# Optimization experiments

Measured on AMD Instinct MI355X. Metric: run time of the kernel, lower is better.

The kernel has to match this reference:

```python
import jax, jax.numpy as jnp
import numpy as np

N_NODES = 50000
N_EDGES = 1_600_000
NUM_GRAPHS = 64
F_NODE = 32
F_EDGE = 16
H = 64
L = 3
BN_EPS = 1e-5


def setup_inputs() -> dict:
    key = jax.random.key(0)
    ks = jax.random.split(key, 20)
    x = jax.random.normal(ks[0], (N_NODES, F_NODE), jnp.float32)
    edge_attr = jax.random.normal(ks[1], (N_EDGES, F_EDGE), jnp.float32)
    edge_index = jax.random.randint(ks[2], (2, N_EDGES), 0, N_NODES, dtype=jnp.int64)
    batch = jnp.sort(jax.random.randint(ks[3], (N_NODES,), 0, NUM_GRAPHS, dtype=jnp.int64))

    def lin(k, fan_in, shape):
        return jax.random.normal(k, shape, jnp.float32) * (1.0 / np.sqrt(fan_in))

    node_W = lin(ks[4], F_NODE, (F_NODE, H));  node_b = jnp.zeros((H,), jnp.float32)
    edge_W = lin(ks[5], F_EDGE, (F_EDGE, H));  edge_b = jnp.zeros((H,), jnp.float32)
    # GINE per-layer MLP: Linear(H, 2H) -> ReLU -> Linear(2H, H)
    W1s = lin(ks[6], H, (L, H, 2 * H));   b1s = jnp.zeros((L, 2 * H), jnp.float32)
    W2s = lin(ks[7], 2 * H, (L, 2 * H, H)); b2s = jnp.zeros((L, H), jnp.float32)
    gammas = jnp.ones((L, H), jnp.float32)
    betas = jnp.zeros((L, H), jnp.float32)
    lin_W = lin(ks[8], H, (H, 1));  lin_b = jnp.zeros((1,), jnp.float32)
    return {
        "x": x, "edge_attr": edge_attr, "edge_index": edge_index, "batch": batch,
        "node_W": node_W, "node_b": node_b, "edge_W": edge_W, "edge_b": edge_b,
        "W1s": W1s, "b1s": b1s, "W2s": W2s, "b2s": b2s,
        "gammas": gammas, "betas": betas, "lin_W": lin_W, "lin_b": lin_b,
    }


def reference(x, edge_attr, edge_index, batch, node_W, node_b, edge_W, edge_b,
              W1s, b1s, W2s, b2s, gammas, betas, lin_W, lin_b):
    # node / edge embeddings
    h = x @ node_W + node_b                  # [N, H]
    e = edge_attr @ edge_W + edge_b          # [E, H]
    src, dst = edge_index[0], edge_index[1]
    for l in range(L):
        # GINEConv (eps=0): m_ij = relu(x_j + e_ij), aggregate sum at target
        m = jax.nn.relu(h[src] + e)                                  # [E, H]
        agg = jax.ops.segment_sum(m, dst, num_segments=N_NODES)     # [N, H]
        z = h + agg
        z = jax.nn.relu(z @ W1s[l] + b1s[l]) @ W2s[l] + b2s[l]       # GINE MLP
        # BatchNorm (training-mode batch stats, biased variance) + ReLU
        mu = jnp.mean(z, axis=0)
        var = jnp.var(z, axis=0)
        h = jax.nn.relu(gammas[l] * (z - mu) * jax.lax.rsqrt(var + BN_EPS) + betas[l])
    # global mean pool per graph
    counts = jax.ops.segment_sum(jnp.ones((N_NODES,), h.dtype), batch, num_segments=NUM_GRAPHS)
    gsum = jax.ops.segment_sum(h, batch, num_segments=NUM_GRAPHS)   # [G, H]
    graph_x = gsum / jnp.maximum(counts, 1.0)[:, None]
    return graph_x @ lin_W + lin_b                                   # [G, 1]
```

## Files before the change

kernel.cpp:

```cpp
#include <hip/hip_runtime.h>

#define NN 50000
#define NE 1600000
#define NG 64
#define HD 64
#define BN_EPS 1e-5f
#define NTILES ((NN + 31) / 32)

typedef unsigned short ushort_t;
typedef unsigned int uint_t;
typedef __attribute__((ext_vector_type(8))) short bf16x8;
typedef __attribute__((ext_vector_type(4))) float f32x4;

__device__ __forceinline__ float b2f(ushort_t u) {
  union { uint_t i; float f; } v; v.i = ((uint_t)u) << 16; return v.f;
}
__device__ __forceinline__ ushort_t f2b(float f) {
  union { float f; uint_t i; } v; v.f = f;
  uint_t x = v.i;
  return (ushort_t)((x + 0x7fffu + ((x >> 16) & 1u)) >> 16);
}
__device__ __forceinline__ uint_t packsplit(float f) {
  ushort_t hi = f2b(f);
  float r = f - b2f(hi);
  ushort_t lo = f2b(r);
  return (uint_t)hi | ((uint_t)lo << 16);
}
__device__ __forceinline__ float LDF(const void* p, int i, int isb) {
  return isb ? b2f(((const ushort_t*)p)[i]) : ((const float*)p)[i];
}
__device__ __forceinline__ int LDI(const void* p, int i, int is64) {
  return is64 ? ((const int*)p)[2 * i] : ((const int*)p)[i];
}
__device__ __forceinline__ int clampi(int v, int hi) {
  return (v < 0) ? 0 : (v >= hi ? hi - 1 : v);
}

__global__ void detect_k(const uint_t* __restrict__ xw, const uint_t* __restrict__ ew,
                         int* __restrict__ flags) {
  int t = threadIdx.x;
  uint_t w = xw[t];
  uint_t b = (w >> 8) & 0x7fu;
  unsigned long long m1 = __ballot(b >= 0x3au && b <= 0x42u);
  unsigned long long m2 = __ballot(ew[2 * t + 1] == 0u);
  if (t == 0) {
    flags[0] = (__popcll(m1) >= 32) ? 1 : 0;
    flags[1] = (__popcll(m2) >= 56) ? 1 : 0;
  }
}

__global__ void __launch_bounds__(256) node_embed(
    const void* __restrict__ x, const void* __restrict__ W,
    const void* __restrict__ b, float* __restrict__ h, const int* __restrict__ flags) {
  __shared__ float xs[64 * 32];
  int isb = flags[0];
  int t = threadIdx.x;
  int base = blockIdx.x * 64;
  int nodes = NN - base; if (nodes > 64) nodes = 64;
  int idx = t * 8;
  if (idx < nodes * 32) {
    if (isb) {
      const uint4* p = (const uint4*)((const ushort_t*)x + base * 32);
      uint4 u = p[t];
      ushort_t* pu = (ushort_t*)&u;
      #pragma unroll
      for (int q = 0; q < 8; q++) xs[idx + q] = b2f(pu[q]);
    } else {
      const float4* p = (const float4*)((const float*)x + base * 32);
      float4 a = p[2 * t], d = p[2 * t + 1];
      xs[idx + 0] = a.x; xs[idx + 1] = a.y; xs[idx + 2] = a.z; xs[idx + 3] = a.w;
      xs[idx + 4] = d.x; xs[idx + 5] = d.y; xs[idx + 6] = d.z; xs[idx + 7] = d.w;
    }
  }
  int c = t & 63, s0 = t >> 6;
  float w[32];
  #pragma unroll
  for (int k = 0; k < 32; k++) w[k] = LDF(W, k * 64 + c, isb);
  float bc = LDF(b, c, isb);
  __syncthreads();
  #pragma unroll 4
  for (int i = 0; i < 16; i++) {
    int slot = s0 * 16 + i;
    int node = base + slot;
    if (node < NN) {
      float acc = bc;
      #pragma unroll
      for (int k = 0; k < 32; k++) acc += xs[slot * 32 + k] * w[k];
      h[node * 64 + c] = acc;
    }
  }
}

__global__ void __launch_bounds__(256) hist_k(
    const void* __restrict__ eidx, int* __restrict__ hist, const int* __restrict__ flags) {
  int is64 = flags[1];
  int e = blockIdx.x * 256 + threadIdx.x;
  if (e >= NE) return;
  int d = clampi(LDI(eidx, NE + e, is64), NN);
  atomicAdd(&hist[d], 1);
}

__global__ void __launch_bounds__(1024) scan_k(
    const int* __restrict__ hist, int* __restrict__ offs) {
  __shared__ int buf[1024];
  int t = threadIdx.x;
  int beg = t * 49, end = beg + 49; if (end > NN) end = NN; if (beg > NN) beg = NN;
  int s = 0;
  for (int i = beg; i < end; i++) s += hist[i];
  buf[t] = s;
  __syncthreads();
  for (int d = 1; d < 1024; d <<= 1) {
    int x = (t >= d) ? buf[t - d] : 0;
    __syncthreads();
    buf[t] += x;
    __syncthreads();
  }
  int run = buf[t] - s;
  for (int i = beg; i < end; i++) { int hv = hist[i]; offs[i] = run; run += hv; }
  if (t == 1023) offs[NN] = run;
}

__global__ void __launch_bounds__(256) scatter_k(
    const void* __restrict__ eidx, int* __restrict__ cursor,
    int* __restrict__ perm, int* __restrict__ psrc, int* __restrict__ pdst,
    const int* __restrict__ flags) {
  int is64 = flags[1];
  int e = blockIdx.x * 256 + threadIdx.x;
  if (e >= NE) return;
  int d = clampi(LDI(eidx, NE + e, is64), NN);
  int s = clampi(LDI(eidx, e, is64), NN);
  int pos = atomicAdd(&cursor[d], 1);
  perm[pos] = e;
  psrc[pos] = s;
  pdst[pos] = d;
}

__global__ void __launch_bounds__(256) pack_eattr(
    const void* __restrict__ eattr, const int* __restrict__ perm,
    ushort_t* __restrict__ phi, ushort_t* __restrict__ plo,
    const int* __restrict__ flags) {
  int isb = flags[0];
  int pos = blockIdx.x * 256 + threadIdx.x;
  if (pos >= NE) return;
  int e = perm[pos];
  int tile = pos >> 4, r = pos & 15;
  union U8 { ushort_t s[8]; uint4 u; };
  if (isb) {
    const uint4* p = (const uint4*)((const ushort_t*)eattr + (size_t)e * 16);
    uint4 h0 = p[0], h1 = p[1];
    ((uint4*)phi)[tile * 32 + r] = h0;
    ((uint4*)phi)[tile * 32 + 16 + r] = h1;
  } else {
    const float4* p = (const float4*)((const float*)eattr + (size_t)e * 16);
    U8 hi[2], lo[2];
    #pragma unroll
    for (int q = 0; q < 4; q++) {
      float4 v = p[q];
      float vv[4] = {v.x, v.y, v.z, v.w};
      #pragma unroll
      for (int j = 0; j < 4; j++) {
        int idx = q * 4 + j;
        ushort_t hb = f2b(vv[j]);
        hi[idx >> 3].s[idx & 7] = hb;
        lo[idx >> 3].s[idx & 7] = f2b(vv[j] - b2f(hb));
      }
    }
    ((uint4*)phi)[tile * 32 + r] = hi[0].u;
    ((uint4*)phi)[tile * 32 + 16 + r] = hi[1].u;
    ((uint4*)plo)[tile * 32 + r] = lo[0].u;
    ((uint4*)plo)[tile * 32 + 16 + r] = lo[1].u;
  }
}

__global__ void __launch_bounds__(256) edge_mfma(
    const ushort_t* __restrict__ phi, const ushort_t* __restrict__ plo,
    const int* __restrict__ psrc, const int* __restrict__ pdst,
    const uint4* __restrict__ wfrag, const float* __restrict__ h,
    float* __restrict__ agg, const int* __restrict__ flags) {
  __shared__ float es[64 * 65];
  __shared__ int ss[64], sd[64];
  int isb = flags[0];
  int t = threadIdx.x;
  int base = blockIdx.x * 64;
  if (t < 64) ss[t] = psrc[base + t];
  else if (t < 128) sd[t - 64] = pdst[base + t - 64];
  int w = t >> 6, lane = t & 63, kg = lane >> 4, cr = lane & 15;
  int tile = blockIdx.x * 4 + w;
  union FR { uint4 u; bf16x8 v; };
  FR ahi, alo;
  ahi.u = make_uint4(0u, 0u, 0u, 0u);
  alo.u = ahi.u;
  if (kg < 2) {
    ahi.u = ((const uint4*)phi)[tile * 32 + kg * 16 + cr];
    if (!isb) alo.u = ((const uint4*)plo)[tile * 32 + kg * 16 + cr];
  }
  f32x4 acc[4];
  #pragma unroll
  for (int nt = 0; nt < 4; nt++) acc[nt] = (f32x4){0.f, 0.f, 0.f, 0.f};
  #pragma unroll
  for (int nt = 0; nt < 4; nt++) {
    FR bh; bh.u = wfrag[nt * 64 + lane];
    acc[nt] = __builtin_amdgcn_mfma_f32_16x16x32_bf16(ahi.v, bh.v, acc[nt], 0, 0, 0);
    if (!isb) {
      FR bl; bl.u = wfrag[256 + nt * 64 + lane];
      acc[nt] = __builtin_amdgcn_mfma_f32_16x16x32_bf16(ahi.v, bl.v, acc[nt], 0, 0, 0);
      acc[nt] = __builtin_amdgcn_mfma_f32_16x16x32_bf16(alo.v, bh.v, acc[nt], 0, 0, 0);
    }
  }
  const float* ebias = (const float*)(wfrag + 512);
  #pragma unroll
  for (int nt = 0; nt < 4; nt++) {
    float bv = ebias[nt * 16 + cr];
    #pragma unroll
    for (int r = 0; r < 4; r++)
      es[(w * 16 + kg * 4 + r) * 65 + nt * 16 + cr] = acc[nt][r] + bv;
  }
  __syncthreads();
  int c = lane, s0 = w;
  float accr = 0.f;
  int cur = -1;
  for (int i = 0; i < 16; i++) {
    int slot = s0 * 16 + i;
    int sn = ss[slot], dn = sd[slot];
    float m = h[(size_t)sn * 64 + c] + es[slot * 65 + c];
    m = m > 0.f ? m : 0.f;
    if (dn != cur) {
      if (cur >= 0) atomicAdd(&agg[cur * 64 + c], accr);
      cur = dn; accr = 0.f;
    }
    accr += m;
  }
  if (cur >= 0) atomicAdd(&agg[cur * 64 + c], accr);
}

__global__ void __launch_bounds__(256) edge_sorted(
    const void* __restrict__ eattr, const int* __restrict__ perm,
    const int* __restrict__ psrc, const int* __restrict__ pdst,
    const void* __restrict__ eW, const void* __restrict__ eb,
    const float* __restrict__ h, float* __restrict__ agg, const int* __restrict__ flags) {
  __shared__ float ea[64 * 16];
  __shared__ int ss[64], sd[64];
  int isb = flags[0];
  int t = threadIdx.x;
  int base = blockIdx.x * 64;
  if (t < 64) ss[t] = psrc[base + t];
  else if (t < 128) sd[t - 64] = pdst[base + t - 64];
  {
    int slot = t >> 2, q = t & 3;
    int pe = perm[base + slot];
    if (isb) {
      const uint2* p = (const uint2*)((const ushort_t*)eattr + (size_t)pe * 16 + q * 4);
      uint2 u = *p;
      ea[slot * 16 + q * 4 + 0] = b2f((ushort_t)(u.x & 0xffffu));
      ea[slot * 16 + q * 4 + 1] = b2f((ushort_t)(u.x >> 16));
      ea[slot * 16 + q * 4 + 2] = b2f((ushort_t)(u.y & 0xffffu));
      ea[slot * 16 + q * 4 + 3] = b2f((ushort_t)(u.y >> 16));
    } else {
      const float4* p = (const float4*)((const float*)eattr + (size_t)pe * 16 + q * 4);
      float4 v = *p;
      ea[slot * 16 + q * 4 + 0] = v.x;
      ea[slot * 16 + q * 4 + 1] = v.y;
      ea[slot * 16 + q * 4 + 2] = v.z;
      ea[slot * 16 + q * 4 + 3] = v.w;
    }
  }
  int c = t & 63, s0 = t >> 6;
  float w[16];
  #pragma unroll
  for (int k = 0; k < 16; k++) w[k] = LDF(eW, k * 64 + c, isb);
  float bc = LDF(eb, c, isb);
  __syncthreads();
  float acc = 0.f;
  int cur = -1;
  for (int i = 0; i < 16; i++) {
    int slot = s0 * 16 + i;
    int sn = ss[slot], dn = sd[slot];
    float e = bc;
    #pragma unroll
    for (int k = 0; k < 16; k++) e += ea[slot * 16 + k] * w[k];
    float m = h[sn * 64 + c] + e;
    m = m > 0.f ? m : 0.f;
    if (dn != cur) {
      if (cur >= 0) atomicAdd(&agg[cur * 64 + c], acc);
      cur = dn; acc = 0.f;
    }
    acc += m;
  }
  if (cur >= 0) atomicAdd(&agg[cur * 64 + c], acc);
}

__global__ void __launch_bounds__(256) prep_w(
    const void* __restrict__ W1s, const void* __restrict__ W2s,
    const void* __restrict__ eW, const void* __restrict__ eB,
    uint4* __restrict__ wpk, const int* __restrict__ flags) {
  int l = blockIdx.x, t = threadIdx.x, isb = flags[0];
  union U8 { ushort_t s[8]; uint4 u; };
  if (l == 3) {
    uint4* wfrag = wpk + 3 * 4096;
    int nt = t >> 6, lane = t & 63;
    int col = nt * 16 + (lane & 15);
    U8 hi, lo;
    #pragma unroll
    for (int j = 0; j < 8; j++) {
      int k = (lane >> 4) * 8 + j;
      float wf = (k < 16) ? LDF(eW, k * 64 + col, isb) : 0.f;
      ushort_t hb = f2b(wf);
      hi.s[j] = hb;
      lo.s[j] = f2b(wf - b2f(hb));
    }
    wfrag[nt * 64 + lane] = hi.u;
    wfrag[256 + nt * 64 + lane] = lo.u;
    if (t < 64) ((float*)(wfrag + 512))[t] = LDF(eB, t, isb);
    return;
  }
  uint4* w1hi = wpk + (size_t)l * 4096;
  uint4* w1lo = w1hi + 1024;
  uint4* w2hi = w1hi + 2048;
  uint4* w2lo = w1hi + 3072;
  for (int o = t; o < 1024; o += 256) {
    int lane = o & 63, f = (o >> 6) & 7, hh = o >> 9;
    int q = lane >> 4, m = lane & 15;
    {
      int kc = f >> 2, i = f & 3;
      U8 hi, lo;
      #pragma unroll
      for (int j = 0; j < 8; j++) {
        int idx = l * 8192 + (kc * 32 + q * 8 + j) * 128 + (hh * 4 + i) * 16 + m;
        float wf = LDF(W1s, idx, isb);
        ushort_t hb = f2b(wf);
        hi.s[j] = hb;
        lo.s[j] = f2b(wf - b2f(hb));
      }
      w1hi[o] = hi.u;
      w1lo[o] = lo.u;
    }
    {
      int kc = f >> 1, i = f & 1;
      U8 hi, lo;
      #pragma unroll
      for (int j = 0; j < 8; j++) {
        int idx = l * 8192 + (kc * 32 + q * 8 + j) * 64 + (hh * 2 + i) * 16 + m;
        float wf = LDF(W2s, idx, isb);
        ushort_t hb = f2b(wf);
        hi.s[j] = hb;
        lo.s[j] = f2b(wf - b2f(hb));
      }
      w2hi[o] = hi.u;
      w2lo[o] = lo.u;
    }
  }
}

__global__ void __launch_bounds__(256) mlp_mfma(
    const float* __restrict__ h, const float* agg,
    const uint4* __restrict__ wpk, const void* __restrict__ b1s,
    const void* __restrict__ b2s,
    float* z2out, float* __restrict__ bnsum, const int* __restrict__ flags, int layer) {
  __shared__ uint_t zs[32 * 65];
  __shared__ uint_t a1s[32 * 129];
  int isb = flags[0];
  int t = threadIdx.x;
  int w = t >> 6, lane = t & 63, q = lane >> 4, m = lane & 15;
  int mt = w & 1;
  int hh = w >> 1;
  int ng1 = hh * 4;
  int ng2 = hh * 2;
  int b1off = layer * 128, b2off = layer * 64;
  const uint4* w1hi = wpk + (size_t)layer * 4096;
  const uint4* w1lo = w1hi + 1024;
  const uint4* w2hi = w1hi + 2048;
  const uint4* w2lo = w1hi + 3072;

  union FR { uint4 u; bf16x8 v; };
  FR w1f[4][2], w2f[2][4];
  #pragma unroll
  for (int kc = 0; kc < 2; kc++)
    #pragma unroll
    for (int i = 0; i < 4; i++)
      w1f[i][kc].u = w1hi[(hh * 8 + kc * 4 + i) * 64 + lane];
  #pragma unroll
  for (int kc = 0; kc < 4; kc++)
    #pragma unroll
    for (int i = 0; i < 2; i++)
      w2f[i][kc].u = w2hi[(hh * 8 + kc * 2 + i) * 64 + lane];

  float b1v[4], b2v[2];
  #pragma unroll
  for (int i = 0; i < 4; i++) b1v[i] = LDF(b1s, b1off + (ng1 + i) * 16 + m, isb);
  #pragma unroll
  for (int i = 0; i < 2; i++) b2v[i] = LDF(b2s, b2off + (ng2 + i) * 16 + m, isb);

  int srow = t >> 3, scol = (t & 7) * 8;
  float ps[2] = {0.f, 0.f}, pq[2] = {0.f, 0.f};

  for (int tile = blockIdx.x; tile < NTILES; tile += gridDim.x) {
    int base = tile * 32;
    __syncthreads();
    {
      int gr = base + srow;
      if (gr < NN) {
        const float4* hp = (const float4*)(h + (size_t)gr * 64 + scol);
        const float4* ap = (const float4*)(agg + (size_t)gr * 64 + scol);
        float4 h0 = hp[0], h1 = hp[1], a0 = ap[0], a1 = ap[1];
        zs[srow * 65 + scol + 0] = packsplit(h0.x + a0.x);
        zs[srow * 65 + scol + 1] = packsplit(h0.y + a0.y);
        zs[srow * 65 + scol + 2] = packsplit(h0.z + a0.z);
        zs[srow * 65 + scol + 3] = packsplit(h0.w + a0.w);
        zs[srow * 65 + scol + 4] = packsplit(h1.x + a1.x);
        zs[srow * 65 + scol + 5] = packsplit(h1.y + a1.y);
        zs[srow * 65 + scol + 6] = packsplit(h1.z + a1.z);
        zs[srow * 65 + scol + 7] = packsplit(h1.w + a1.w);
      } else {
        #pragma unroll
        for (int jj = 0; jj < 8; jj++) zs[srow * 65 + scol + jj] = 0;
      }
    }
    __syncthreads();
    f32x4 acc1[4];
    #pragma unroll
    for (int i = 0; i < 4; i++) acc1[i] = (f32x4){0.f, 0.f, 0.f, 0.f};
    #pragma unroll
    for (int kc = 0; kc < 2; kc++) {
      int ab = (mt * 16 + m) * 65 + kc * 32 + q * 8;
      bf16x8 ahi, alo;
      #pragma unroll
      for (int j = 0; j < 8; j++) {
        uint_t u = zs[ab + j];
        ahi[j] = (short)(u & 0xffffu);
        alo[j] = (short)(u >> 16);
      }
      #pragma unroll
      for (int i = 0; i < 4; i++) {
        acc1[i] = __builtin_amdgcn_mfma_f32_16x16x32_bf16(ahi, w1f[i][kc].v, acc1[i], 0, 0, 0);
        acc1[i] = __builtin_amdgcn_mfma_f32_16x16x32_bf16(alo, w1f[i][kc].v, acc1[i], 0, 0, 0);
        if (!isb) {
          FR bl;
          bl.u = w1lo[(hh * 8 + kc * 4 + i) * 64 + lane];
          acc1[i] = __builtin_amdgcn_mfma_f32_16x16x32_bf16(ahi, bl.v, acc1[i], 0, 0, 0);
        }
      }
    }
    #pragma unroll
    for (int i = 0; i < 4; i++) {
      #pragma unroll
      for (int r = 0; r < 4; r++) {
        float v = acc1[i][r] + b1v[i];
        v = v > 0.f ? v : 0.f;
        a1s[(mt * 16 + q * 4 + r) * 129 + (ng1 + i) * 16 + m] = packsplit(v);
      }
    }
    __syncthreads();
    f32x4 acc2[2];
    #pragma unroll
    for (int i = 0; i < 2; i++) acc2[i] = (f32x4){0.f, 0.f, 0.f, 0.f};
    #pragma unroll
    for (int kc = 0; kc < 4; kc++) {
      int ab = (mt * 16 + m) * 129 + kc * 32 + q * 8;
      bf16x8 ahi, alo;
      #pragma unroll
      for (int j = 0; j < 8; j++) {
        uint_t u = a1s[ab + j];
        ahi[j] = (short)(u & 0xffffu);
        alo[j] = (short)(u >> 16);
      }
      #pragma unroll
      for (int i = 0; i < 2; i++) {
        acc2[i] = __builtin_amdgcn_mfma_f32_16x16x32_bf16(ahi, w2f[i][kc].v, acc2[i], 0, 0, 0);
        acc2[i] = __builtin_amdgcn_mfma_f32_16x16x32_bf16(alo, w2f[i][kc].v, acc2[i], 0, 0, 0);
        if (!isb) {
          FR bl;
          bl.u = w2lo[(hh * 8 + kc * 2 + i) * 64 + lane];
          acc2[i] = __builtin_amdgcn_mfma_f32_16x16x32_bf16(ahi, bl.v, acc2[i], 0, 0, 0);
        }
      }
    }
    #pragma unroll
    for (int i = 0; i < 2; i++) {
      int col = (ng2 + i) * 16 + m;
      #pragma unroll
      for (int r = 0; r < 4; r++) {
        int gr = base + mt * 16 + q * 4 + r;
        if (gr < NN) {
          float v = acc2[i][r] + b2v[i];
          z2out[(size_t)gr * 64 + col] = v;
          ps[i] += v; pq[i] += v * v;
        }
      }
    }
  }
  __syncthreads();
  float* red = (float*)zs;
  if (t < 128) red[t] = 0.f;
  __syncthreads();
  #pragma unroll
  for (int i = 0; i < 2; i++) {
    int col = (ng2 + i) * 16 + m;
    atomicAdd(&red[col], ps[i]);
    atomicAdd(&red[64 + col], pq[i]);
  }
  __syncthreads();
  if (t < 128) atomicAdd(&bnsum[t], red[t]);
}

__global__ void bn_fin(const float* __restrict__ bnsum, const void* __restrict__ gammas,
                       const void* __restrict__ betas, float* __restrict__ scsh,
                       const int* __restrict__ flags, int layer) {
  int c = threadIdx.x;
  int isb = flags[0];
  float inv_n = 1.0f / (float)NN;
  float mu = bnsum[c] * inv_n;
  float var = bnsum[64 + c] * inv_n - mu * mu;
  var = var > 0.f ? var : 0.f;
  float sc = LDF(gammas, layer * 64 + c, isb) * rsqrtf(var + BN_EPS);
  scsh[c] = sc;
  scsh[64 + c] = LDF(betas, layer * 64 + c, isb) - mu * sc;
}

__global__ void __launch_bounds__(256) bn_apply(
    const float* __restrict__ z2, const float* __restrict__ scsh, float* __restrict__ h) {
  int t = blockIdx.x * 256 + threadIdx.x;
  if (t < NN * 16) {
    float4 z = ((const float4*)z2)[t];
    int c4 = t & 15;
    float4 sc = ((const float4*)scsh)[c4];
    float4 sh = ((const float4*)(scsh + 64))[c4];
    float4 r;
    r.x = fmaxf(z.x * sc.x + sh.x, 0.f);
    r.y = fmaxf(z.y * sc.y + sh.y, 0.f);
    r.z = fmaxf(z.z * sc.z + sh.z, 0.f);
    r.w = fmaxf(z.w * sc.w + sh.w, 0.f);
    ((float4*)h)[t] = r;
  }
}

__global__ void __launch_bounds__(256) find_bounds(
    const void* __restrict__ batch, int* __restrict__ bounds, const int* __restrict__ flags) {
  int is64 = flags[1];
  int i = blockIdx.x * 256 + threadIdx.x;
  if (i >= NN) return;
  int cur = clampi(LDI(batch, i, is64), NG);
  if (i == 0) {
    for (int g = 0; g <= cur; g++) bounds[g] = 0;
  } else {
    int prev = clampi(LDI(batch, i - 1, is64), NG);
    for (int g = prev + 1; g <= cur; g++) bounds[g] = i;
  }
  if (i == NN - 1) {
    for (int g = cur + 1; g <= NG; g++) bounds[g] = NN;
  }
}

__global__ void __launch_bounds__(256) pool_final(
    const float* __restrict__ h, const int* __restrict__ bounds,
    const void* __restrict__ linW, const void* __restrict__ linB,
    float* __restrict__ out, const int* __restrict__ flags) {
  __shared__ float red[4][64];
  int isb = flags[0];
  int g = blockIdx.x;
  int t = threadIdx.x, c = t & 63, w = t >> 6;
  int s = bounds[g], e = bounds[g + 1];
  float acc = 0.f;
  for (int i = s + w; i < e; i += 4) acc += h[i * 64 + c];
  red[w][c] = acc;
  __syncthreads();
  if (t < 64) {
    float v = red[0][c] + red[1][c] + red[2][c] + red[3][c];
    float cnt = (float)(e - s); if (cnt < 1.f) cnt = 1.f;
    v = (v / cnt) * LDF(linW, c, isb);
    #pragma unroll
    for (int m = 32; m >= 1; m >>= 1) v += __shfl_xor(v, m, 64);
    if (c == 0) out[g] = v + LDF(linB, 0, isb);
  }
}

extern "C" void kernel_launch(void* const* d_in, const int* in_sizes, int n_in,
                              void* d_out, int out_size, void* d_ws, size_t ws_size,
                              hipStream_t stream) {
  const void* x     = d_in[0];
  const void* eattr = d_in[1];
  const void* eidx  = d_in[2];
  const void* batch = d_in[3];
  const void* nodeW = d_in[4];
  const void* nodeB = d_in[5];
  const void* edgeW = d_in[6];
  const void* edgeB = d_in[7];
  const void* W1s   = d_in[8];
  const void* b1s   = d_in[9];
  const void* W2s   = d_in[10];
  const void* b2s   = d_in[11];
  const void* gam   = d_in[12];
  const void* bet   = d_in[13];
  const void* linW  = d_in[14];
  const void* linB  = d_in[15];
  float* out = (float*)d_out;

  int*   flags  = (int*)d_ws;
  float* h      = (float*)d_ws + 16;
  float* agg    = h + (size_t)NN * HD;
  float* bnsum  = agg + (size_t)NN * HD;
  float* scsh   = bnsum + 128;
  int*   bounds = (int*)(scsh + 128);
  int*   offs   = bounds + 80;
  int*   cursor = offs + (NN + 1);
  int*   perm   = cursor + (NN + 1);
  int*   psrc   = perm + NE;
  int*   pdst   = psrc + NE;

  size_t base_words = 16ull + 2ull * NN * HD + 128 + 128 + 80;
  size_t sort_words = base_words + 2ull * (NN + 1) + 3ull * NE;
  size_t wpk_words_start = (sort_words + 3ull) & ~3ull;
  size_t wpk_words = (3ull * 4096 + 528) * 4;
  size_t needed = (wpk_words_start + wpk_words) * 4ull;
  if (ws_size < needed) return;
  uint4* wpk = (uint4*)((float*)d_ws + wpk_words_start);
  uint4* wfrag = wpk + 3ull * 4096;
  size_t z2_start = wpk_words_start + wpk_words;
  float* z2sep = (float*)d_ws + z2_start;
  int have_z2 = ws_size >= (z2_start + (size_t)NN * HD) * 4ull;
  float* z2 = have_z2 ? z2sep : agg;
  size_t pat_start = z2_start + (size_t)NN * HD;
  size_t pat_words = (size_t)NE * 8;
  int have_pat = have_z2 && (ws_size >= (pat_start + 2ull * pat_words) * 4ull);
  ushort_t* phi = (ushort_t*)((float*)d_ws + pat_start);
  ushort_t* plo = (ushort_t*)((float*)d_ws + pat_start + pat_words);

  detect_k<<<1, 64, 0, stream>>>((const uint_t*)x, (const uint_t*)eidx, flags);
  prep_w<<<4, 256, 0, stream>>>(W1s, W2s, edgeW, edgeB, wpk, flags);
  node_embed<<<(NN + 63) / 64, 256, 0, stream>>>(x, nodeW, nodeB, h, flags);

  hipMemsetAsync(offs, 0, (NN + 1) * sizeof(int), stream);
  hist_k<<<NE / 256, 256, 0, stream>>>(eidx, offs, flags);
  scan_k<<<1, 1024, 0, stream>>>(offs, cursor);
  scatter_k<<<NE / 256, 256, 0, stream>>>(eidx, cursor, perm, psrc, pdst, flags);
  if (have_pat)
    pack_eattr<<<NE / 256, 256, 0, stream>>>(eattr, perm, phi, plo, flags);

  for (int l = 0; l < 3; l++) {
    hipMemsetAsync(agg, 0, (size_t)NN * HD * sizeof(float), stream);
    if (have_pat)
      edge_mfma<<<NE / 64, 256, 0, stream>>>(phi, plo, psrc, pdst, wfrag, h, agg, flags);
    else
      edge_sorted<<<NE / 64, 256, 0, stream>>>(eattr, perm, psrc, pdst, edgeW, edgeB, h, agg, flags);
    hipMemsetAsync(bnsum, 0, 128 * sizeof(float), stream);
    mlp_mfma<<<784, 256, 0, stream>>>(h, agg, wpk, b1s, b2s, z2, bnsum, flags, l);
    bn_fin<<<1, 64, 0, stream>>>(bnsum, gam, bet, scsh, flags, l);
    bn_apply<<<3125, 256, 0, stream>>>(z2, scsh, h);
  }
  find_bounds<<<(NN + 255) / 256, 256, 0, stream>>>(batch, bounds, flags);
  pool_final<<<NG, 256, 0, stream>>>(h, bounds, linW, linB, out, flags);
}
```

Measured before the change: 1.081 ms.

## Bucket edges by source range and pin buckets to XCDs for L2 locality

Edges are now sorted by a composite key of source-node bucket (8 buckets of 6250 nodes) and destination, and each bucket is padded to 64-edge chunks. The edge kernel maps blockIdx&7 to a bucket so each XCD gathers h rows from one source range, meant to keep those gathers resident in that XCD's L2. The per-thread h gathers are also hoisted into a register array so the loads can be issued together. In exchange, the histogram and scan work over 8x more bins, padding edges need masking, and destinations repeat across buckets, so segmented runs are shorter and more atomics are issued.

```diff
diff --git a/kernel.cpp b/kernel.cpp
--- a/kernel.cpp
+++ b/kernel.cpp
@@ -6,6 +6,11 @@
 #define HD 64
 #define BN_EPS 1e-5f
 #define NTILES ((NN + 31) / 32)
+#define NBUCK 8
+#define NPB 6250
+#define NBINS (NBUCK * NN)
+#define NEP (NE + 512)
+#define SLOTS 3584
 
 typedef unsigned short ushort_t;
 typedef unsigned int uint_t;
@@ -97,17 +102,48 @@
   int e = blockIdx.x * 256 + threadIdx.x;
   if (e >= NE) return;
   int d = clampi(LDI(eidx, NE + e, is64), NN);
-  atomicAdd(&hist[d], 1);
+  int s = clampi(LDI(eidx, e, is64), NN);
+  int bin = (s / NPB) * NN + d;
+  atomicAdd(&hist[bin], 1);
 }
 
 __global__ void __launch_bounds__(1024) scan_k(
-    const int* __restrict__ hist, int* __restrict__ offs) {
+    const int* __restrict__ hist, int* __restrict__ starts, int* __restrict__ meta) {
   __shared__ int buf[1024];
+  __shared__ int sA[NBUCK + 1];
+  __shared__ int sT[NBUCK];
+  __shared__ int sPT[NBUCK];
   int t = threadIdx.x;
-  int beg = t * 49, end = beg + 49; if (end > NN) end = NN; if (beg > NN) beg = NN;
-  int s = 0;
-  for (int i = beg; i < end; i++) s += hist[i];
-  buf[t] = s;
+  int active = t < 1000;
+  const int4* h4 = (const int4*)hist;
+  int4* s4 = (int4*)starts;
+  int ssum = 0;
+  if (active) {
+    for (int i = t * 100; i < t * 100 + 100; i++) {
+      int4 v = h4[i];
+      ssum += v.x + v.y + v.z + v.w;
+    }
+  }
+  buf[t] = ssum;
+  __syncthreads();
+  if (t < NBUCK) {
+    int T = 0;
+    for (int i = t * 125; i < t * 125 + 125; i++) T += buf[i];
+    sT[t] = T;
+  }
+  __syncthreads();
+  if (t == 0) {
+    int a = 0, pt = 0;
+    for (int b = 0; b < NBUCK; b++) {
+      sA[b] = a; sPT[b] = pt;
+      meta[b] = a;
+      meta[16 + b] = a + sT[b];
+      pt += sT[b];
+      a = (a + sT[b] + 63) & ~63;
+    }
+    sA[NBUCK] = a;
+    meta[NBUCK] = a;
+  }
   __syncthreads();
   for (int d = 1; d < 1024; d <<= 1) {
     int x = (t >= d) ? buf[t - d] : 0;
@@ -115,9 +151,30 @@
     buf[t] += x;
     __syncthreads();
   }
-  int run = buf[t] - s;
-  for (int i = beg; i < end; i++) { int hv = hist[i]; offs[i] = run; run += hv; }
-  if (t == 1023) offs[NN] = run;
+  if (active) {
+    int b = t / 125;
+    int run = sA[b] + (buf[t] - ssum - sPT[b]);
+    for (int i = t * 100; i < t * 100 + 100; i++) {
+      int4 v = h4[i];
+      int4 o;
+      o.x = run; run += v.x;
+      o.y = run; run += v.y;
+      o.z = run; run += v.z;
+      o.w = run; run += v.w;
+      s4[i] = o;
+    }
+  }
+}
+
+__global__ void pad_fill(const int* __restrict__ meta, int* __restrict__ perm,
+                         int* __restrict__ psrc, int* __restrict__ pdst) {
+  int t = threadIdx.x;
+  for (int b = 0; b < NBUCK; b++) {
+    int re = meta[16 + b], ae = meta[b + 1];
+    for (int p = re + t; p < ae; p += 64) {
+      perm[p] = 0; psrc[p] = 0; pdst[p] = NN;
+    }
+  }
 }
 
 __global__ void __launch_bounds__(256) scatter_k(
@@ -129,7 +186,8 @@
   if (e >= NE) return;
   int d = clampi(LDI(eidx, NE + e, is64), NN);
   int s = clampi(LDI(eidx, e, is64), NN);
-  int pos = atomicAdd(&cursor[d], 1);
+  int bin = (s / NPB) * NN + d;
+  int pos = atomicAdd(&cursor[bin], 1);
   perm[pos] = e;
   psrc[pos] = s;
   pdst[pos] = d;
@@ -138,10 +196,10 @@
 __global__ void __launch_bounds__(256) pack_eattr(
     const void* __restrict__ eattr, const int* __restrict__ perm,
     ushort_t* __restrict__ phi, ushort_t* __restrict__ plo,
-    const int* __restrict__ flags) {
+    const int* __restrict__ flags, const int* __restrict__ meta) {
   int isb = flags[0];
   int pos = blockIdx.x * 256 + threadIdx.x;
-  if (pos >= NE) return;
+  if (pos >= meta[8]) return;
   int e = perm[pos];
   int tile = pos >> 4, r = pos & 15;
   union U8 { ushort_t s[8]; uint4 u; };
@@ -176,16 +234,35 @@
     const ushort_t* __restrict__ phi, const ushort_t* __restrict__ plo,
     const int* __restrict__ psrc, const int* __restrict__ pdst,
     const uint4* __restrict__ wfrag, const float* __restrict__ h,
-    float* __restrict__ agg, const int* __restrict__ flags) {
-  __shared__ float es[64 * 65];
+    float* __restrict__ agg, const int* __restrict__ flags,
+    const int* __restrict__ meta) {
+  __shared__ float es[64 * 68];
   __shared__ int ss[64], sd[64];
+  int A[9];
+  #pragma unroll
+  for (int b = 0; b < 9; b++) A[b] = meta[b];
+  int maxcb = 0;
+  #pragma unroll
+  for (int b = 0; b < NBUCK; b++) {
+    int cb = (A[b + 1] - A[b]) >> 6;
+    maxcb = cb > maxcb ? cb : maxcb;
+  }
+  int chunk;
+  if (maxcb <= SLOTS) {
+    int xcd = blockIdx.x & 7, s = blockIdx.x >> 3;
+    if (s >= ((A[xcd + 1] - A[xcd]) >> 6)) return;
+    chunk = (A[xcd] >> 6) + s;
+  } else {
+    chunk = blockIdx.x;
+    if (chunk * 64 >= A[8]) return;
+  }
+  int base = chunk * 64;
   int isb = flags[0];
   int t = threadIdx.x;
-  int base = blockIdx.x * 64;
   if (t < 64) ss[t] = psrc[base + t];
   else if (t < 128) sd[t - 64] = pdst[base + t - 64];
   int w = t >> 6, lane = t & 63, kg = lane >> 4, cr = lane & 15;
-  int tile = blockIdx.x * 4 + w;
+  int tile = chunk * 4 + w;
   union FR { uint4 u; bf16x8 v; };
   FR ahi, alo;
   ahi.u = make_uint4(0u, 0u, 0u, 0u);
@@ -213,36 +290,43 @@
     float bv = ebias[nt * 16 + cr];
     #pragma unroll
     for (int r = 0; r < 4; r++)
-      es[(w * 16 + kg * 4 + r) * 65 + nt * 16 + cr] = acc[nt][r] + bv;
+      es[(w * 16 + kg * 4 + r) * 68 + nt * 16 + cr] = acc[nt][r] + bv;
   }
   __syncthreads();
   int c = lane, s0 = w;
+  float hv[16];
+  #pragma unroll
+  for (int i = 0; i < 16; i++)
+    hv[i] = h[(size_t)ss[s0 * 16 + i] * 64 + c];
   float accr = 0.f;
   int cur = -1;
+  #pragma unroll
   for (int i = 0; i < 16; i++) {
     int slot = s0 * 16 + i;
-    int sn = ss[slot], dn = sd[slot];
-    float m = h[(size_t)sn * 64 + c] + es[slot * 65 + c];
+    int dn = sd[slot];
+    float m = hv[i] + es[slot * 68 + c];
     m = m > 0.f ? m : 0.f;
     if (dn != cur) {
-      if (cur >= 0) atomicAdd(&agg[cur * 64 + c], accr);
+      if (cur >= 0 && cur < NN) atomicAdd(&agg[cur * 64 + c], accr);
       cur = dn; accr = 0.f;
     }
     accr += m;
   }
-  if (cur >= 0) atomicAdd(&agg[cur * 64 + c], accr);
+  if (cur >= 0 && cur < NN) atomicAdd(&agg[cur * 64 + c], accr);
 }
 
 __global__ void __launch_bounds__(256) edge_sorted(
     const void* __restrict__ eattr, const int* __restrict__ perm,
     const int* __restrict__ psrc, const int* __restrict__ pdst,
     const void* __restrict__ eW, const void* __restrict__ eb,
-    const float* __restrict__ h, float* __restrict__ agg, const int* __restrict__ flags) {
+    const float* __restrict__ h, float* __restrict__ agg,
+    const int* __restrict__ flags, const int* __restrict__ meta) {
   __shared__ float ea[64 * 16];
   __shared__ int ss[64], sd[64];
   int isb = flags[0];
   int t = threadIdx.x;
   int base = blockIdx.x * 64;
+  if (base >= meta[8]) return;
   if (t < 64) ss[t] = psrc[base + t];
   else if (t < 128) sd[t - 64] = pdst[base + t - 64];
   {
@@ -281,12 +365,12 @@
     float m = h[sn * 64 + c] + e;
     m = m > 0.f ? m : 0.f;
     if (dn != cur) {
-      if (cur >= 0) atomicAdd(&agg[cur * 64 + c], acc);
+      if (cur >= 0 && cur < NN) atomicAdd(&agg[cur * 64 + c], acc);
       cur = dn; acc = 0.f;
     }
     acc += m;
   }
-  if (cur >= 0) atomicAdd(&agg[cur * 64 + c], acc);
+  if (cur >= 0 && cur < NN) atomicAdd(&agg[cur * 64 + c], acc);
 }
 
 __global__ void __launch_bounds__(256) prep_w(
@@ -595,20 +679,21 @@
   float* out = (float*)d_out;
 
   int*   flags  = (int*)d_ws;
-  float* h      = (float*)d_ws + 16;
+  int*   meta   = flags + 16;
+  float* h      = (float*)(meta + 48);
   float* agg    = h + (size_t)NN * HD;
   float* bnsum  = agg + (size_t)NN * HD;
   float* scsh   = bnsum + 128;
   int*   bounds = (int*)(scsh + 128);
   int*   offs   = bounds + 80;
-  int*   cursor = offs + (NN + 1);
-  int*   perm   = cursor + (NN + 1);
-  int*   psrc   = perm + NE;
-  int*   pdst   = psrc + NE;
-
-  size_t base_words = 16ull + 2ull * NN * HD + 128 + 128 + 80;
-  size_t sort_words = base_words + 2ull * (NN + 1) + 3ull * NE;
-  size_t wpk_words_start = (sort_words + 3ull) & ~3ull;
+  int*   cursor = offs + NBINS;
+  int*   perm   = cursor + NBINS;
+  int*   psrc   = perm + NEP;
+  int*   pdst   = psrc + NEP;
+
+  size_t base_words = 64ull + 2ull * NN * HD + 128 + 128 + 80
+                    + 2ull * NBINS + 3ull * NEP;
+  size_t wpk_words_start = (base_words + 3ull) & ~3ull;
   size_t wpk_words = (3ull * 4096 + 528) * 4;
   size_t needed = (wpk_words_start + wpk_words) * 4ull;
   if (ws_size < needed) return;
@@ -619,7 +704,7 @@
   int have_z2 = ws_size >= (z2_start + (size_t)NN * HD) * 4ull;
   float* z2 = have_z2 ? z2sep : agg;
   size_t pat_start = z2_start + (size_t)NN * HD;
-  size_t pat_words = (size_t)NE * 8;
+  size_t pat_words = (size_t)NEP * 8;
   int have_pat = have_z2 && (ws_size >= (pat_start + 2ull * pat_words) * 4ull);
   ushort_t* phi = (ushort_t*)((float*)d_ws + pat_start);
   ushort_t* plo = (ushort_t*)((float*)d_ws + pat_start + pat_words);
@@ -628,20 +713,21 @@
   prep_w<<<4, 256, 0, stream>>>(W1s, W2s, edgeW, edgeB, wpk, flags);
   node_embed<<<(NN + 63) / 64, 256, 0, stream>>>(x, nodeW, nodeB, h, flags);
 
-  hipMemsetAsync(offs, 0, (NN + 1) * sizeof(int), stream);
+  hipMemsetAsync(offs, 0, (size_t)NBINS * sizeof(int), stream);
   hist_k<<<NE / 256, 256, 0, stream>>>(eidx, offs, flags);
-  scan_k<<<1, 1024, 0, stream>>>(offs, cursor);
+  scan_k<<<1, 1024, 0, stream>>>(offs, cursor, meta);
+  pad_fill<<<1, 64, 0, stream>>>(meta, perm, psrc, pdst);
   scatter_k<<<NE / 256, 256, 0, stream>>>(eidx, cursor, perm, psrc, pdst, flags);
   if (have_pat)
-    pack_eattr<<<NE / 256, 256, 0, stream>>>(eattr, perm, phi, plo, flags);
+    pack_eattr<<<NEP / 256, 256, 0, stream>>>(eattr, perm, phi, plo, flags, meta);
 
   for (int l = 0; l < 3; l++) {
     hipMemsetAsync(agg, 0, (size_t)NN * HD * sizeof(float), stream);
     if (have_pat)
-      edge_mfma<<<NE / 64, 256, 0, stream>>>(phi, plo, psrc, pdst, wfrag, h, agg, flags);
+      edge_mfma<<<8 * SLOTS, 256, 0, stream>>>(phi, plo, psrc, pdst, wfrag, h, agg, flags, meta);
     else
-      edge_sorted<<<NE / 64, 256, 0, stream>>>(eattr, perm, psrc, pdst, edgeW, edgeB, h, agg, flags);
-    hipMemsetAsync(bnsum, 0, 128 * sizeof(float), stream);
+      edge_sorted<<<NEP / 64, 256, 0, stream>>>(eattr, perm, psrc, pdst, edgeW, edgeB, h, agg, flags, meta);
+    hipMemsetAsync(bnsum, 0, 128 * sizeof(int), stream);
     mlp_mfma<<<784, 256, 0, stream>>>(h, agg, wpk, b1s, b2s, z2, bnsum, flags, l);
     bn_fin<<<1, 64, 0, stream>>>(bnsum, gam, bet, scsh, flags, l);
     bn_apply<<<3125, 256, 0, stream>>>(z2, scsh, h);
```

Result: no change. 1.099 ms (+1.6%).
